# Performance work log

Hardware: AMD Instinct MI355X
Metric: run time of the kernel (lower is better)

The kernel has to match this reference:

```python
import jax, jax.numpy as jnp
import numpy as np

EPS = 1e-12  # torch F.normalize default eps


def setup_inputs() -> dict:
    key = jax.random.key(0)
    k1, k2, k3, k4 = jax.random.split(key, 4)
    N, F_IN, F_OUT = 8192, 128, 128
    x = jax.random.normal(k1, (N, F_IN), dtype=jnp.float32)
    adj = jax.random.uniform(k2, (N, N), dtype=jnp.float32)
    # fc_layer params (xavier_uniform with relu gain for W, default-ish bias)
    gain = float(np.sqrt(2.0))
    limit = gain * float(np.sqrt(6.0 / (F_IN + F_OUT)))
    W = jax.random.uniform(k3, (F_OUT, F_IN), dtype=jnp.float32, minval=-limit, maxval=limit)
    b = jax.random.uniform(k4, (F_OUT,), dtype=jnp.float32, minval=-1.0 / np.sqrt(F_IN), maxval=1.0 / np.sqrt(F_IN))
    return {"x": x, "adj": adj, "W": W, "b": b}


def reference(x, adj, W, b):
    N = adj.shape[0]
    # A' = A + I (self loops)
    a = adj + jnp.eye(N, dtype=adj.dtype)
    # degree normalization D^-1/2 A' D^-1/2 as a fused broadcast scale
    # (the torch code does this via two dense diag matmuls; same math)
    dinv = jax.lax.rsqrt(jnp.sum(a, axis=-1))  # [N]
    a = a * dinv[:, None] * dinv[None, :]
    # aggregation + linear
    h = a @ x                    # [N, F_IN]
    h = h @ W.T + b              # [N, F_OUT]
    # F.normalize(dim=1): L2 normalize each row
    norm = jnp.linalg.norm(h, axis=1, keepdims=True)
    return h / jnp.maximum(norm, EPS)
```

## Files before the change

### kernel.cpp

```cpp
#include <hip/hip_runtime.h>
#include <hip/hip_bf16.h>


typedef __attribute__((ext_vector_type(8))) short short8;
typedef __attribute__((ext_vector_type(4))) float f32x4;
typedef __attribute__((ext_vector_type(4))) unsigned short us4;

static __device__ __forceinline__ unsigned short f2bf(float f) {
    unsigned int u = __float_as_uint(f);
    u += 0x7FFFu + ((u >> 16) & 1u);
    return (unsigned short)(u >> 16);
}

__global__ __launch_bounds__(256) void gcn_prep(
    const float* __restrict__ adj, const float* __restrict__ x,
    const float* __restrict__ W,
    unsigned short* __restrict__ yT, float* __restrict__ dinv,
    unsigned short* __restrict__ Wb)
{
    const int tid = threadIdx.x;
    const int blk = blockIdx.x;
    if (blk >= 8192) {
        int idx = (blk - 8192) * 256 + tid;
        Wb[idx] = f2bf(W[idx]);
        return;
    }
    const long j = blk;
    const float4* row = (const float4*)(adj + j * 8192L);
    float s = 0.f;
#pragma unroll
    for (int it = 0; it < 8; ++it) {
        float4 v = row[it * 256 + tid];
        s += v.x + v.y + v.z + v.w;
    }
    for (int off = 1; off < 64; off <<= 1) s += __shfl_xor(s, off, 64);
    __shared__ float ps[4];
    __shared__ float sdi;
    if ((tid & 63) == 0) ps[tid >> 6] = s;
    __syncthreads();
    if (tid == 0) {
        float tot = ps[0] + ps[1] + ps[2] + ps[3] + 1.0f;
        float di = rsqrtf(tot);
        dinv[j] = di;
        sdi = di;
    }
    __syncthreads();
    if (tid < 128) {
        yT[(long)tid * 8192 + j] = f2bf(sdi * x[j * 128 + tid]);
    }
}

#define M_TILE 32
#define BKC    512
#define NCHUNK 16

__global__ __launch_bounds__(256, 1) void gcn_main(
    const float* __restrict__ adj, const float* __restrict__ x,
    const float* __restrict__ bias,
    const unsigned short* __restrict__ yT, const float* __restrict__ dinv,
    const unsigned short* __restrict__ Wb, float* __restrict__ out)
{
    __shared__ unsigned short Ab[2][M_TILE][BKC];

    const int tid  = threadIdx.x;
    const int wave = tid >> 6;
    const int lane = tid & 63;
    const int q    = lane >> 4;
    const int ln   = lane & 15;
    const int nb   = wave * 32;
    const long rowBase = (long)blockIdx.x * M_TILE;

    f32x4 acc[2][2] = {};
    float4 st[16];

    auto load_chunk = [&](int c) {
#pragma unroll
        for (int i = 0; i < 16; ++i) {
            int t   = wave * 16 + i;
            int row = t >> 1;
            int col = ((t & 1) << 8) + (lane << 2);
            st[i] = *(const float4*)&adj[(rowBase + row) * 8192L + (long)c * BKC + col];
        }
    };
    auto write_chunk = [&](int buf) {
#pragma unroll
        for (int i = 0; i < 16; ++i) {
            int t   = wave * 16 + i;
            int row = t >> 1;
            int col = ((t & 1) << 8) + (lane << 2);
            us4 w4;
            w4.x = f2bf(st[i].x); w4.y = f2bf(st[i].y);
            w4.z = f2bf(st[i].z); w4.w = f2bf(st[i].w);
            *(us4*)&Ab[buf][row][col] = w4;
        }
    };

    load_chunk(0);
    write_chunk(0);
    __syncthreads();

#pragma unroll 1
    for (int c = 0; c < NCHUNK; ++c) {
        const int cur = c & 1;
        if (c + 1 < NCHUNK) load_chunk(c + 1);
#pragma unroll 4
        for (int s = 0; s < BKC / 32; ++s) {
            const int k0 = s * 32 + q * 8;
            short8 a0 = *(const short8*)&Ab[cur][ln][k0];
            short8 a1 = *(const short8*)&Ab[cur][16 + ln][k0];
            const long kg = (long)c * BKC + k0;
            short8 b0 = *(const short8*)&yT[(nb + ln) * 8192L + kg];
            short8 b1 = *(const short8*)&yT[(nb + 16 + ln) * 8192L + kg];
            acc[0][0] = __builtin_amdgcn_mfma_f32_16x16x32_bf16(a0, b0, acc[0][0], 0, 0, 0);
            acc[0][1] = __builtin_amdgcn_mfma_f32_16x16x32_bf16(a0, b1, acc[0][1], 0, 0, 0);
            acc[1][0] = __builtin_amdgcn_mfma_f32_16x16x32_bf16(a1, b0, acc[1][0], 0, 0, 0);
            acc[1][1] = __builtin_amdgcn_mfma_f32_16x16x32_bf16(a1, b1, acc[1][1], 0, 0, 0);
        }
        if (c + 1 < NCHUNK) write_chunk(cur ^ 1);
        __syncthreads();
    }

    unsigned short* t_lds = &Ab[0][0][0];
    float* s_dinv = (float*)(t_lds + 32 * 136);
    float* s_part = s_dinv + 32;
    float* s_inv  = s_part + 128;

    if (tid < 32) s_dinv[tid] = dinv[rowBase + tid];
    __syncthreads();

#pragma unroll
    for (int mi = 0; mi < 2; ++mi)
#pragma unroll
        for (int nj = 0; nj < 2; ++nj)
#pragma unroll
            for (int r = 0; r < 4; ++r) {
                int m = mi * 16 + q * 4 + r;
                int n = nb + nj * 16 + ln;
                float di = s_dinv[m];
                float tv = di * acc[mi][nj][r] + di * di * x[(rowBase + m) * 128 + n];
                t_lds[m * 136 + n] = f2bf(tv);
            }
    __syncthreads();

    f32x4 z[2][2] = {};
#pragma unroll
    for (int s = 0; s < 4; ++s) {
        const int k0 = s * 32 + q * 8;
        short8 a0 = *(const short8*)&t_lds[ln * 136 + k0];
        short8 a1 = *(const short8*)&t_lds[(16 + ln) * 136 + k0];
        short8 b0 = *(const short8*)&Wb[(nb + ln) * 128 + k0];
        short8 b1 = *(const short8*)&Wb[(nb + 16 + ln) * 128 + k0];
        z[0][0] = __builtin_amdgcn_mfma_f32_16x16x32_bf16(a0, b0, z[0][0], 0, 0, 0);
        z[0][1] = __builtin_amdgcn_mfma_f32_16x16x32_bf16(a0, b1, z[0][1], 0, 0, 0);
        z[1][0] = __builtin_amdgcn_mfma_f32_16x16x32_bf16(a1, b0, z[1][0], 0, 0, 0);
        z[1][1] = __builtin_amdgcn_mfma_f32_16x16x32_bf16(a1, b1, z[1][1], 0, 0, 0);
    }

    float bv0 = bias[nb + ln], bv1 = bias[nb + 16 + ln];
    float zv[2][2][4];
    float rp[2][4];
#pragma unroll
    for (int mi = 0; mi < 2; ++mi)
#pragma unroll
        for (int r = 0; r < 4; ++r) {
            float v0 = z[mi][0][r] + bv0;
            float v1 = z[mi][1][r] + bv1;
            zv[mi][0][r] = v0; zv[mi][1][r] = v1;
            rp[mi][r] = v0 * v0 + v1 * v1;
        }
#pragma unroll
    for (int mi = 0; mi < 2; ++mi)
#pragma unroll
        for (int r = 0; r < 4; ++r)
            for (int off = 1; off < 16; off <<= 1)
                rp[mi][r] += __shfl_xor(rp[mi][r], off, 64);
    if (ln == 0) {
#pragma unroll
        for (int mi = 0; mi < 2; ++mi)
#pragma unroll
            for (int r = 0; r < 4; ++r)
                s_part[(mi * 16 + q * 4 + r) * 4 + wave] = rp[mi][r];
    }
    __syncthreads();
    if (tid < 32) {
        float s = s_part[tid * 4] + s_part[tid * 4 + 1] + s_part[tid * 4 + 2] + s_part[tid * 4 + 3];
        float nrm = sqrtf(s);
        s_inv[tid] = 1.0f / fmaxf(nrm, 1e-12f);
    }
    __syncthreads();

#pragma unroll
    for (int mi = 0; mi < 2; ++mi)
#pragma unroll
        for (int nj = 0; nj < 2; ++nj)
#pragma unroll
            for (int r = 0; r < 4; ++r) {
                int m = mi * 16 + q * 4 + r;
                int n = nb + nj * 16 + ln;
                out[(rowBase + m) * 128 + n] = zv[mi][nj][r] * s_inv[m];
            }
}

extern "C" void kernel_launch(void* const* d_in, const int* in_sizes, int n_in,
                              void* d_out, int out_size, void* d_ws, size_t ws_size,
                              hipStream_t stream) {
    const float* x   = (const float*)d_in[0];
    const float* adj = (const float*)d_in[1];
    const float* W   = (const float*)d_in[2];
    const float* b   = (const float*)d_in[3];
    float* out = (float*)d_out;

    unsigned short* yT  = (unsigned short*)d_ws;
    float*          dv  = (float*)((char*)d_ws + (2u << 20));
    unsigned short* Wb  = (unsigned short*)((char*)d_ws + (2u << 20) + 32768);

    gcn_prep<<<8192 + 64, 256, 0, stream>>>(adj, x, W, yT, dv, Wb);
    gcn_main<<<256, 256, 0, stream>>>(adj, x, b, yT, dv, Wb, out);
}
```

Before: 476.5 us.

## Pre-convert adjacency to bf16 and stream it into LDS with async loads

The prep kernel now writes a bf16 copy of the adjacency while computing degrees. The main kernel streams that copy straight into LDS with global_load_lds, using an XOR swizzle, instead of loading fp32 into registers and converting there. Building the scaled, transposed x and the bf16 W moves into a separate kernel that stages through LDS, so the yT writes are coalesced. Total adjacency traffic stays about the same, since the fp32 read plus bf16 write replaces the second fp32 read. The change adds a 128MB workspace buffer and one more kernel launch.

New measurement: 483.3 us. About the same (+1.4%).

```diff
diff --git a/kernel.cpp b/kernel.cpp
--- a/kernel.cpp
+++ b/kernel.cpp
@@ -12,42 +12,64 @@
     return (unsigned short)(u >> 16);
 }
 
+static __device__ __forceinline__ void gload_lds16(const void* g, void* l) {
+    __builtin_amdgcn_global_load_lds(
+        (const __attribute__((address_space(1))) unsigned int*)g,
+        (__attribute__((address_space(3))) unsigned int*)l, 16, 0, 0);
+}
+
 __global__ __launch_bounds__(256) void gcn_prep(
-    const float* __restrict__ adj, const float* __restrict__ x,
-    const float* __restrict__ W,
-    unsigned short* __restrict__ yT, float* __restrict__ dinv,
-    unsigned short* __restrict__ Wb)
+    const float* __restrict__ adj, unsigned short* __restrict__ adjb,
+    float* __restrict__ dinv)
 {
     const int tid = threadIdx.x;
-    const int blk = blockIdx.x;
-    if (blk >= 8192) {
-        int idx = (blk - 8192) * 256 + tid;
-        Wb[idx] = f2bf(W[idx]);
-        return;
-    }
-    const long j = blk;
+    const long j = blockIdx.x;
     const float4* row = (const float4*)(adj + j * 8192L);
+    us4* brow = (us4*)(adjb + j * 8192L);
     float s = 0.f;
 #pragma unroll
     for (int it = 0; it < 8; ++it) {
         float4 v = row[it * 256 + tid];
         s += v.x + v.y + v.z + v.w;
+        us4 w;
+        w.x = f2bf(v.x); w.y = f2bf(v.y); w.z = f2bf(v.z); w.w = f2bf(v.w);
+        brow[it * 256 + tid] = w;
     }
     for (int off = 1; off < 64; off <<= 1) s += __shfl_xor(s, off, 64);
     __shared__ float ps[4];
-    __shared__ float sdi;
     if ((tid & 63) == 0) ps[tid >> 6] = s;
     __syncthreads();
-    if (tid == 0) {
-        float tot = ps[0] + ps[1] + ps[2] + ps[3] + 1.0f;
-        float di = rsqrtf(tot);
-        dinv[j] = di;
-        sdi = di;
-    }
-    __syncthreads();
-    if (tid < 128) {
-        yT[(long)tid * 8192 + j] = f2bf(sdi * x[j * 128 + tid]);
-    }
+    if (tid == 0)
+        dinv[j] = rsqrtf(ps[0] + ps[1] + ps[2] + ps[3] + 1.0f);
+}
+
+__global__ __launch_bounds__(256) void gcn_build(
+    const float* __restrict__ x, const float* __restrict__ W,
+    const float* __restrict__ dinv,
+    unsigned short* __restrict__ yT, unsigned short* __restrict__ Wb)
+{
+    __shared__ float xs[64][129];
+    __shared__ float sd[64];
+    const int tid = threadIdx.x;
+    const long j0 = (long)blockIdx.x * 64;
+    if (blockIdx.x == 0)
+        for (int i = tid; i < 16384; i += 256) Wb[i] = f2bf(W[i]);
+    if (tid < 64) sd[tid] = dinv[j0 + tid];
+    const float4* xg = (const float4*)(x + j0 * 128);
+#pragma unroll
+    for (int it = 0; it < 8; ++it) {
+        int idx = it * 256 + tid;
+        int r = idx >> 5, c4 = idx & 31;
+        float4 v = xg[idx];
+        xs[r][c4 * 4 + 0] = v.x; xs[r][c4 * 4 + 1] = v.y;
+        xs[r][c4 * 4 + 2] = v.z; xs[r][c4 * 4 + 3] = v.w;
+    }
+    __syncthreads();
+    const int jj = tid & 63, fg = tid >> 6;
+    const float d = sd[jj];
+#pragma unroll
+    for (int f = fg; f < 128; f += 4)
+        yT[(long)f * 8192 + j0 + jj] = f2bf(d * xs[jj][f]);
 }
 
 #define M_TILE 32
@@ -55,7 +77,7 @@
 #define NCHUNK 16
 
 __global__ __launch_bounds__(256, 1) void gcn_main(
-    const float* __restrict__ adj, const float* __restrict__ x,
+    const unsigned short* __restrict__ adjb, const float* __restrict__ x,
     const float* __restrict__ bias,
     const unsigned short* __restrict__ yT, const float* __restrict__ dinv,
     const unsigned short* __restrict__ Wb, float* __restrict__ out)
@@ -71,53 +93,41 @@
     const long rowBase = (long)blockIdx.x * M_TILE;
 
     f32x4 acc[2][2] = {};
-    float4 st[16];
-
-    auto load_chunk = [&](int c) {
-#pragma unroll
-        for (int i = 0; i < 16; ++i) {
-            int t   = wave * 16 + i;
-            int row = t >> 1;
-            int col = ((t & 1) << 8) + (lane << 2);
-            st[i] = *(const float4*)&adj[(rowBase + row) * 8192L + (long)c * BKC + col];
+
+    auto issue = [&](int c, int buf) {
+#pragma unroll
+        for (int i = 0; i < 8; ++i) {
+            int r = wave * 8 + i;
+            const unsigned short* g =
+                adjb + (rowBase + r) * 8192L + (long)c * BKC + ((lane ^ (r & 7)) << 3);
+            gload_lds16(g, &Ab[buf][r][0]);
         }
     };
-    auto write_chunk = [&](int buf) {
-#pragma unroll
-        for (int i = 0; i < 16; ++i) {
-            int t   = wave * 16 + i;
-            int row = t >> 1;
-            int col = ((t & 1) << 8) + (lane << 2);
-            us4 w4;
-            w4.x = f2bf(st[i].x); w4.y = f2bf(st[i].y);
-            w4.z = f2bf(st[i].z); w4.w = f2bf(st[i].w);
-            *(us4*)&Ab[buf][row][col] = w4;
-        }
-    };
-
-    load_chunk(0);
-    write_chunk(0);
-    __syncthreads();
+
+    issue(0, 0);
+
+    const unsigned short* bp0 = yT + (long)(nb + ln) * 8192;
+    const unsigned short* bp1 = bp0 + 16 * 8192L;
+    const int swz = ln & 7;
 
 #pragma unroll 1
     for (int c = 0; c < NCHUNK; ++c) {
         const int cur = c & 1;
-        if (c + 1 < NCHUNK) load_chunk(c + 1);
+        __syncthreads();
+        if (c + 1 < NCHUNK) issue(c + 1, cur ^ 1);
 #pragma unroll 4
         for (int s = 0; s < BKC / 32; ++s) {
-            const int k0 = s * 32 + q * 8;
-            short8 a0 = *(const short8*)&Ab[cur][ln][k0];
-            short8 a1 = *(const short8*)&Ab[cur][16 + ln][k0];
-            const long kg = (long)c * BKC + k0;
-            short8 b0 = *(const short8*)&yT[(nb + ln) * 8192L + kg];
-            short8 b1 = *(const short8*)&yT[(nb + 16 + ln) * 8192L + kg];
+            const int cb = (((s * 4 + q) ^ swz) << 3);
+            short8 a0 = *(const short8*)&Ab[cur][ln][cb];
+            short8 a1 = *(const short8*)&Ab[cur][16 + ln][cb];
+            const long kg = (long)c * BKC + s * 32 + q * 8;
+            short8 b0 = *(const short8*)&bp0[kg];
+            short8 b1 = *(const short8*)&bp1[kg];
             acc[0][0] = __builtin_amdgcn_mfma_f32_16x16x32_bf16(a0, b0, acc[0][0], 0, 0, 0);
             acc[0][1] = __builtin_amdgcn_mfma_f32_16x16x32_bf16(a0, b1, acc[0][1], 0, 0, 0);
             acc[1][0] = __builtin_amdgcn_mfma_f32_16x16x32_bf16(a1, b0, acc[1][0], 0, 0, 0);
             acc[1][1] = __builtin_amdgcn_mfma_f32_16x16x32_bf16(a1, b1, acc[1][1], 0, 0, 0);
         }
-        if (c + 1 < NCHUNK) write_chunk(cur ^ 1);
-        __syncthreads();
     }
 
     unsigned short* t_lds = &Ab[0][0][0];
@@ -183,9 +193,8 @@
     }
     __syncthreads();
     if (tid < 32) {
-        float s = s_part[tid * 4] + s_part[tid * 4 + 1] + s_part[tid * 4 + 2] + s_part[tid * 4 + 3];
-        float nrm = sqrtf(s);
-        s_inv[tid] = 1.0f / fmaxf(nrm, 1e-12f);
+        float ssum = s_part[tid * 4] + s_part[tid * 4 + 1] + s_part[tid * 4 + 2] + s_part[tid * 4 + 3];
+        s_inv[tid] = 1.0f / fmaxf(sqrtf(ssum), 1e-12f);
     }
     __syncthreads();
 
@@ -210,10 +219,13 @@
     const float* b   = (const float*)d_in[3];
     float* out = (float*)d_out;
 
-    unsigned short* yT  = (unsigned short*)d_ws;
-    float*          dv  = (float*)((char*)d_ws + (2u << 20));
-    unsigned short* Wb  = (unsigned short*)((char*)d_ws + (2u << 20) + 32768);
-
-    gcn_prep<<<8192 + 64, 256, 0, stream>>>(adj, x, W, yT, dv, Wb);
-    gcn_main<<<256, 256, 0, stream>>>(adj, x, b, yT, dv, Wb, out);
-}
+    char* ws = (char*)d_ws;
+    unsigned short* adjb = (unsigned short*)ws;
+    unsigned short* yT   = (unsigned short*)(ws + (134217728L));
+    float*          dv   = (float*)(ws + 134217728L + (2L << 20));
+    unsigned short* Wb   = (unsigned short*)(ws + 134217728L + (2L << 20) + 32768);
+
+    gcn_prep <<<8192, 256, 0, stream>>>(adj, adjb, dv);
+    gcn_build<<<128,  256, 0, stream>>>(x, W, dv, yT, Wb);
+    gcn_main <<<256,  256, 0, stream>>>(adjb, x, b, yT, dv, Wb, out);
+}
```
